# Optimization experiments

Hardware: AMD Instinct MI355X
Metric: run time of the kernel (lower is better)

The kernel has to match this reference:

```python
import jax, jax.numpy as jnp
import numpy as np

NUM_EMBEDDINGS = 1024
EMBEDDING_DIM = 512
B, H, W = 32, 32, 32


def setup_inputs() -> dict:
    key = jax.random.key(0)
    k1, k2 = jax.random.split(key)
    z = jax.random.normal(k1, (B, EMBEDDING_DIM, H, W), dtype=jnp.float32)
    embedding = jax.random.normal(k2, (NUM_EMBEDDINGS, EMBEDDING_DIM), dtype=jnp.float32)
    return {"z": z, "embedding": embedding}


def reference(z, embedding):
    # z: [B, C, H, W] -> [B, H, W, C] -> [N, C]
    zp = jnp.transpose(z, (0, 2, 3, 1))
    b, h, w, d = zp.shape
    z_flat = zp.reshape(-1, d)
    # squared L2 distances: ||z||^2 - 2 z e^T + ||e||^2  -> [N, K]
    distances = (
        jnp.sum(z_flat ** 2, axis=1, keepdims=True)
        - 2.0 * (z_flat @ embedding.T)
        + jnp.sum(embedding ** 2, axis=1)
    )
    indices = jnp.argmin(distances, axis=1)  # [N]
    # one-hot @ embedding == direct gather
    quantized = embedding[indices]  # [N, d]
    quantized = quantized.reshape(b, h, w, d).transpose(0, 3, 1, 2)  # [B, C, H, W]
    return quantized, 0.0, indices.reshape(b, -1)
```

## Files before the change

### kernel.cpp

```cpp
#include <hip/hip_runtime.h>
#include <cfloat>

typedef _Float16 half8 __attribute__((ext_vector_type(8)));
typedef float    f32x4 __attribute__((ext_vector_type(4)));
typedef unsigned int  uint;
typedef unsigned short ushort;

constexpr int DIM  = 512;
constexpr int NEMB = 1024;
constexpr int HW   = 1024;
constexpr int NROW = 32 * HW;

constexpr long long QCOUNT = (long long)32 * 512 * 32 * 32;
constexpr long long SOFF   = QCOUNT;
constexpr long long IOFF   = SOFF + 1;

constexpr size_t WS_ZT    = 0;
constexpr size_t WS_ET    = 33554432;
constexpr size_t WS_ENORM = 34603008;
constexpr size_t WS_CNT   = 34607104;
constexpr size_t WS_LIST  = 34607360;
constexpr size_t WS_CANDB = WS_LIST + (size_t)NROW * 4;
constexpr size_t WS_CANDI = WS_CANDB + (size_t)2 * NROW * 8;
constexpr size_t WS_NEED  = WS_CANDI + (size_t)2 * NROW * 4;

constexpr float DELTA = 0.25f;

__device__ __forceinline__ void gld16(const void* g, void* l) {
    __builtin_amdgcn_global_load_lds(
        (const __attribute__((address_space(1))) void*)g,
        (__attribute__((address_space(3))) void*)l, 16, 0, 0);
}
union PKH8 { half8 v; _Float16 h[8]; };

__device__ __forceinline__ int swz8(int r, int g) {
    return g ^ (r & 7);
}

__global__ __launch_bounds__(256) void prep(const float* __restrict__ z,
                                            const float* __restrict__ e,
                                            char* __restrict__ zt,
                                            char* __restrict__ et,
                                            float* __restrict__ enorm,
                                            int* __restrict__ cnt) {
    __shared__ float ls[64][129];
    const int bx = blockIdx.x;
    const int t  = threadIdx.x;
    if (bx >= 2048) {
        const int eb = bx - 2048;
        if (eb == 0 && t == 0) *cnt = 0;
        int gid = eb * 256 + t;
        int ke  = gid >> 6;
        int kbg = gid & 63;
        const float* src = e + (size_t)ke * DIM + kbg * 8;
        PKH8 h;
        float s = 0.f;
        #pragma unroll
        for (int j = 0; j < 8; ++j) {
            float v = src[j];
            h.h[j] = (_Float16)v;
            s += v * v;
        }
        int nc = ke >> 7, r = ke & 127, kc64 = kbg >> 3, g = kbg & 7;
        size_t byte = ((size_t)(nc * 8 + kc64)) * 16384 + (size_t)r * 128
                    + ((size_t)swz8(r, g) << 4);
        *reinterpret_cast<half8*>(et + byte) = h.v;
        #pragma unroll
        for (int off = 32; off > 0; off >>= 1) s += __shfl_down(s, off, 64);
        if (kbg == 0) enorm[ke] = s;
        return;
    }
    const int mb  = bx >> 3, kcc = bx & 7;
    const int b   = mb >> 3;
    const int hw0 = (mb & 7) * 128;
    for (int i = t; i < 64 * 128; i += 256) {
        int c = i >> 7, hw = i & 127;
        ls[c][hw] = z[((size_t)(b * DIM + kcc * 64 + c)) * HW + hw0 + hw];
    }
    __syncthreads();
    for (int j = t; j < 1024; j += 256) {
        int r = j >> 3, g = j & 7;
        PKH8 h;
        #pragma unroll
        for (int jj = 0; jj < 8; ++jj) h.h[jj] = (_Float16)ls[g * 8 + jj][r];
        size_t byte = ((size_t)(mb * 8 + kcc)) * 16384 + (size_t)r * 128
                    + ((size_t)swz8(r, g) << 4);
        *reinterpret_cast<half8*>(zt + byte) = h.v;
    }
}

#define VQ_STAGE(SS, BUF)                                                      \
  {                                                                            \
    const int kc_ = (SS) & 7;                                                  \
    const size_t tB_ = ((size_t)((half4 + ((SS) >> 3)) * 8 + kc_)) * 16384;    \
    char* dst_ = smem + (BUF) * 32768;                                         \
    gld16(zt + zbase + (size_t)kc_ * 16384 + toff,        dst_ + toff);        \
    gld16(zt + zbase + (size_t)kc_ * 16384 + 8192 + toff, dst_ + 8192 + toff); \
    gld16(et + tB_ + toff,        dst_ + 16384 + toff);                        \
    gld16(et + tB_ + 8192 + toff, dst_ + 24576 + toff);                        \
  }

#define VQ_STEP(S, VMLIT, BUF)                                                 \
  {                                                                            \
    asm volatile("s_waitcnt vmcnt(" VMLIT ")" ::: "memory");                   \
    __builtin_amdgcn_s_barrier();                                              \
    const char* buf_ = smem + (BUF) * 32768;                                   \
    half8 a00 = *reinterpret_cast<const half8*>(buf_ + aoff0);                 \
    half8 a01 = *reinterpret_cast<const half8*>(buf_ + aoff1);                 \
    half8 a10 = *reinterpret_cast<const half8*>(buf_ + (aoff0 ^ 64));          \
    half8 a11 = *reinterpret_cast<const half8*>(buf_ + (aoff1 ^ 64));          \
    half8 b00 = *reinterpret_cast<const half8*>(buf_ + 16384 + boff0);         \
    half8 b01 = *reinterpret_cast<const half8*>(buf_ + 16384 + boff1);         \
    half8 b02 = *reinterpret_cast<const half8*>(buf_ + 16384 + boff2);         \
    half8 b03 = *reinterpret_cast<const half8*>(buf_ + 16384 + boff3);         \
    half8 b10 = *reinterpret_cast<const half8*>(buf_ + 16384 + (boff0 ^ 64));  \
    half8 b11 = *reinterpret_cast<const half8*>(buf_ + 16384 + (boff1 ^ 64));  \
    half8 b12 = *reinterpret_cast<const half8*>(buf_ + 16384 + (boff2 ^ 64));  \
    half8 b13 = *reinterpret_cast<const half8*>(buf_ + 16384 + (boff3 ^ 64));  \
    asm volatile("s_waitcnt lgkmcnt(0)" ::: "memory");                         \
    __builtin_amdgcn_sched_barrier(0);                                         \
    __builtin_amdgcn_s_barrier();                                              \
    if ((S) + 2 < 32) VQ_STAGE((S) + 2, BUF);                                  \
    acc[0][0] = __builtin_amdgcn_mfma_f32_16x16x32_f16(a00, b00, acc[0][0], 0, 0, 0); \
    acc[0][1] = __builtin_amdgcn_mfma_f32_16x16x32_f16(a00, b01, acc[0][1], 0, 0, 0); \
    acc[0][2] = __builtin_amdgcn_mfma_f32_16x16x32_f16(a00, b02, acc[0][2], 0, 0, 0); \
    acc[0][3] = __builtin_amdgcn_mfma_f32_16x16x32_f16(a00, b03, acc[0][3], 0, 0, 0); \
    acc[1][0] = __builtin_amdgcn_mfma_f32_16x16x32_f16(a01, b00, acc[1][0], 0, 0, 0); \
    acc[1][1] = __builtin_amdgcn_mfma_f32_16x16x32_f16(a01, b01, acc[1][1], 0, 0, 0); \
    acc[1][2] = __builtin_amdgcn_mfma_f32_16x16x32_f16(a01, b02, acc[1][2], 0, 0, 0); \
    acc[1][3] = __builtin_amdgcn_mfma_f32_16x16x32_f16(a01, b03, acc[1][3], 0, 0, 0); \
    acc[0][0] = __builtin_amdgcn_mfma_f32_16x16x32_f16(a10, b10, acc[0][0], 0, 0, 0); \
    acc[0][1] = __builtin_amdgcn_mfma_f32_16x16x32_f16(a10, b11, acc[0][1], 0, 0, 0); \
    acc[0][2] = __builtin_amdgcn_mfma_f32_16x16x32_f16(a10, b12, acc[0][2], 0, 0, 0); \
    acc[0][3] = __builtin_amdgcn_mfma_f32_16x16x32_f16(a10, b13, acc[0][3], 0, 0, 0); \
    acc[1][0] = __builtin_amdgcn_mfma_f32_16x16x32_f16(a11, b10, acc[1][0], 0, 0, 0); \
    acc[1][1] = __builtin_amdgcn_mfma_f32_16x16x32_f16(a11, b11, acc[1][1], 0, 0, 0); \
    acc[1][2] = __builtin_amdgcn_mfma_f32_16x16x32_f16(a11, b12, acc[1][2], 0, 0, 0); \
    acc[1][3] = __builtin_amdgcn_mfma_f32_16x16x32_f16(a11, b13, acc[1][3], 0, 0, 0); \
    if (((S) & 7) == 7) {                                                      \
      const int ncl_ = ((S) >> 3) * 128;                                       \
      _Pragma("unroll")                                                        \
      for (int n = 0; n < 4; ++n) {                                            \
        const int lcol = ncl_ + wc * 64 + n * 16 + lr;                         \
        const float en = enorm_l[lcol];                                        \
        const int col = half * 512 + lcol;                                     \
        _Pragma("unroll")                                                      \
        for (int m = 0; m < 2; ++m) {                                          \
          _Pragma("unroll")                                                    \
          for (int q = 0; q < 4; ++q) {                                        \
            float dv = en - 2.0f * acc[m][n][q];                               \
            int sl = m * 4 + q;                                                \
            if (dv < b1v[sl]) { b2v[sl] = b1v[sl]; b1v[sl] = dv; i1v[sl] = col; } \
            else if (dv < b2v[sl]) b2v[sl] = dv;                               \
          }                                                                    \
        }                                                                      \
      }                                                                        \
      _Pragma("unroll")                                                        \
      for (int m = 0; m < 2; ++m)                                              \
        _Pragma("unroll")                                                      \
        for (int n = 0; n < 4; ++n) acc[m][n] = (f32x4)(0.f);                  \
    }                                                                          \
  }

__global__ __launch_bounds__(512, 4) void vq_mfma(const char* __restrict__ zt,
                                                  const char* __restrict__ et,
                                                  const float* __restrict__ enorm,
                                                  float2* __restrict__ cand_b,
                                                  int* __restrict__ cand_i) {
    __shared__ __align__(16) char smem[65536];
    __shared__ float enorm_l[512];

    const int t = threadIdx.x;
    const int w = t >> 6, l = t & 63;
    const int lr = l & 15, hg = l >> 4;
    const int wr = w >> 1;
    const int wc = w & 1;
    const int bid = blockIdx.x;
    const int mb = bid >> 1;
    const int half = bid & 1;
    const int half4 = half * 4;
    const int n0 = mb * 128;

    const int swz = swz8(lr, hg) << 4;
    const int aoff0 = (wr * 32 + lr) * 128 + swz;
    const int aoff1 = (wr * 32 + 16 + lr) * 128 + swz;
    const int boff0 = (wc * 64 + lr) * 128 + swz;
    const int boff1 = (wc * 64 + 16 + lr) * 128 + swz;
    const int boff2 = (wc * 64 + 32 + lr) * 128 + swz;
    const int boff3 = (wc * 64 + 48 + lr) * 128 + swz;

    enorm_l[t] = enorm[half * 512 + t];
    if (t + 256 < 512) enorm_l[t + 256] = enorm[half * 512 + t + 256];
    __syncthreads();

    float b1v[8], b2v[8]; int i1v[8];
    #pragma unroll
    for (int s = 0; s < 8; ++s) { b1v[s] = FLT_MAX; b2v[s] = FLT_MAX; i1v[s] = 0; }

    const size_t zbase = (size_t)mb * 8 * 16384;
    const int toff = t * 16;

    f32x4 acc[2][4];
    #pragma unroll
    for (int m = 0; m < 2; ++m)
        #pragma unroll
        for (int n = 0; n < 4; ++n) acc[m][n] = (f32x4)(0.f);

    VQ_STAGE(0, 0);
    VQ_STAGE(1, 1);

    for (int sp = 0; sp < 30; sp += 2) {
        VQ_STEP(sp + 0, "4", 0);
        VQ_STEP(sp + 1, "4", 1);
    }
    VQ_STEP(30, "4", 0);
    VQ_STEP(31, "0", 1);

    #pragma unroll
    for (int s = 0; s < 8; ++s) {
        #pragma unroll
        for (int off = 1; off <= 8; off <<= 1) {
            float ob1 = __shfl_xor(b1v[s], off, 64);
            int   oi1 = __shfl_xor(i1v[s], off, 64);
            float ob2 = __shfl_xor(b2v[s], off, 64);
            if (ob1 < b1v[s] || (ob1 == b1v[s] && oi1 < i1v[s])) {
                b2v[s] = fminf(b1v[s], ob2);
                b1v[s] = ob1; i1v[s] = oi1;
            } else {
                b2v[s] = fminf(b2v[s], ob1);
            }
        }
    }
    __syncthreads();
    float* red_b1 = reinterpret_cast<float*>(smem);
    float* red_b2 = reinterpret_cast<float*>(smem + 1024);
    int*   red_i1 = reinterpret_cast<int*>  (smem + 2048);
    if (lr == 0) {
        #pragma unroll
        for (int s = 0; s < 8; ++s) {
            int row = wr * 32 + (s >> 2) * 16 + hg * 4 + (s & 3);
            red_b1[row * 2 + wc] = b1v[s];
            red_b2[row * 2 + wc] = b2v[s];
            red_i1[row * 2 + wc] = i1v[s];
        }
    }
    __syncthreads();
    if (t < 128) {
        float a1 = red_b1[t * 2], a2 = red_b2[t * 2]; int ai = red_i1[t * 2];
        float c1 = red_b1[t * 2 + 1], c2 = red_b2[t * 2 + 1]; int ci = red_i1[t * 2 + 1];
        float B1, B2; int I1;
        if (c1 < a1 || (c1 == a1 && ci < ai)) { B1 = c1; I1 = ci; B2 = fminf(a1, c2); }
        else                                   { B1 = a1; I1 = ai; B2 = fminf(a2, c1); }
        cand_b[(size_t)half * NROW + n0 + t] = make_float2(B1, B2);
        cand_i[(size_t)half * NROW + n0 + t] = I1;
    }
}

__global__ __launch_bounds__(256) void combine(const float2* __restrict__ cand_b,
                                               const int* __restrict__ cand_i,
                                               const float* __restrict__ e,
                                               float* __restrict__ out,
                                               int* __restrict__ cnt,
                                               int* __restrict__ list) {
    __shared__ int idx_f[64];
    const int t = threadIdx.x;
    const int n0 = blockIdx.x * 64;
    if (t < 64) {
        const int row = n0 + t;
        float2 a = cand_b[row];
        float2 c = cand_b[NROW + row];
        int ai = cand_i[row];
        int ci = cand_i[NROW + row];
        float B1, B2; int I1;
        if (c.x < a.x) { B1 = c.x; I1 = ci; B2 = fminf(a.x, c.y); }
        else           { B1 = a.x; I1 = ai; B2 = fminf(a.y, c.x); }
        idx_f[t] = I1;
        out[IOFF + row] = (float)I1;
        if (B2 - B1 < DELTA) {
            int pos = atomicAdd(cnt, 1);
            list[pos] = row;
        }
    }
    if (blockIdx.x == 0 && t == 0) out[SOFF] = 0.0f;
    __syncthreads();

    const int b   = n0 >> 10;
    const int hw0 = n0 & (HW - 1);
    const int row4 = (t & 15) * 4;
    const int i0 = idx_f[row4 + 0];
    const int i1 = idx_f[row4 + 1];
    const int i2 = idx_f[row4 + 2];
    const int i3 = idx_f[row4 + 3];
    #pragma unroll 4
    for (int p = 0; p < 32; ++p) {
        int c = (t >> 4) + (p << 4);
        float4 v;
        v.x = e[(size_t)i0 * DIM + c];
        v.y = e[(size_t)i1 * DIM + c];
        v.z = e[(size_t)i2 * DIM + c];
        v.w = e[(size_t)i3 * DIM + c];
        *reinterpret_cast<float4*>(&out[((size_t)(b * DIM + c)) * HW + hw0 + row4]) = v;
    }
}

__global__ __launch_bounds__(256) void recheck(const float* __restrict__ z,
                                               const float* __restrict__ e,
                                               const float* __restrict__ enorm,
                                               const int* __restrict__ cnt,
                                               const int* __restrict__ list,
                                               float* __restrict__ out) {
    __shared__ float zrow[4][512];
    __shared__ float rb[256];
    __shared__ int   ri[256];
    __shared__ int   fidx[4];
    const int t = threadIdx.x;
    const int count = *cnt;
    const int ngrp = (count + 3) >> 2;
    for (int g = blockIdx.x; g < ngrp; g += gridDim.x) {
        const int base = g * 4;
        const int nr = min(4, count - base);
        __syncthreads();
        for (int r = 0; r < nr; ++r) {
            const int row = list[base + r];
            const int b = row >> 10, hw = row & (HW - 1);
            zrow[r][t]       = z[((size_t)(b * DIM + t))       * HW + hw];
            zrow[r][t + 256] = z[((size_t)(b * DIM + t + 256)) * HW + hw];
        }
        __syncthreads();
        float best[4]; int bi[4];
        #pragma unroll
        for (int r = 0; r < 4; ++r) { best[r] = FLT_MAX; bi[r] = 0; }
        #pragma unroll
        for (int p = 0; p < 4; ++p) {
            const int ke = t + p * 256;
            const float4* ep = reinterpret_cast<const float4*>(e + (size_t)ke * DIM);
            float d0 = 0.f, d1 = 0.f, d2 = 0.f, d3 = 0.f;
            const float4* z0 = reinterpret_cast<const float4*>(zrow[0]);
            const float4* z1 = reinterpret_cast<const float4*>(zrow[1]);
            const float4* z2 = reinterpret_cast<const float4*>(zrow[2]);
            const float4* z3 = reinterpret_cast<const float4*>(zrow[3]);
            for (int c = 0; c < 128; ++c) {
                float4 ev = ep[c];
                float4 a0 = z0[c], a1 = z1[c], a2 = z2[c], a3 = z3[c];
                d0 += ev.x*a0.x + ev.y*a0.y + ev.z*a0.z + ev.w*a0.w;
                d1 += ev.x*a1.x + ev.y*a1.y + ev.z*a1.z + ev.w*a1.w;
                d2 += ev.x*a2.x + ev.y*a2.y + ev.z*a2.z + ev.w*a2.w;
                d3 += ev.x*a3.x + ev.y*a3.y + ev.z*a3.z + ev.w*a3.w;
            }
            const float en = enorm[ke];
            float dd[4] = { en - 2.f*d0, en - 2.f*d1, en - 2.f*d2, en - 2.f*d3 };
            #pragma unroll
            for (int r = 0; r < 4; ++r)
                if (dd[r] < best[r]) { best[r] = dd[r]; bi[r] = ke; }
        }
        for (int r = 0; r < nr; ++r) {
            rb[t] = best[r]; ri[t] = bi[r];
            __syncthreads();
            #pragma unroll
            for (int s = 128; s > 0; s >>= 1) {
                if (t < s) {
                    float ov = rb[t + s]; int oi = ri[t + s];
                    if (ov < rb[t] || (ov == rb[t] && oi < ri[t])) {
                        rb[t] = ov; ri[t] = oi;
                    }
                }
                __syncthreads();
            }
            if (t == 0) {
                fidx[r] = ri[0];
                out[IOFF + list[base + r]] = (float)ri[0];
            }
            __syncthreads();
        }
        for (int r = 0; r < nr; ++r) {
            const int row = list[base + r];
            const int b = row >> 10, hw = row & (HW - 1);
            const int fbi = fidx[r];
            out[((size_t)(b * DIM + t))       * HW + hw] = e[(size_t)fbi * DIM + t];
            out[((size_t)(b * DIM + t + 256)) * HW + hw] = e[(size_t)fbi * DIM + t + 256];
        }
    }
}

constexpr int TM = 64;
constexpr int TN = 256;
constexpr int KC = 32;
constexpr int ZST = 68;
constexpr int EST = 260;

union F4 { float4 v; float f[4]; };

__global__ __launch_bounds__(256) void enorm_kernel(const float* __restrict__ e,
                                                    float* __restrict__ enorm) {
    int gid  = blockIdx.x * 256 + threadIdx.x;
    int wave = gid >> 6;
    int lane = gid & 63;
    if (wave >= NEMB) return;
    const float* row = e + (size_t)wave * DIM;
    float4 a = *reinterpret_cast<const float4*>(row + lane * 8);
    float4 b = *reinterpret_cast<const float4*>(row + lane * 8 + 4);
    float s = a.x*a.x + a.y*a.y + a.z*a.z + a.w*a.w
            + b.x*b.x + b.y*b.y + b.z*b.z + b.w*b.w;
    #pragma unroll
    for (int off = 32; off > 0; off >>= 1) s += __shfl_down(s, off, 64);
    if (lane == 0) enorm[wave] = s;
}

__global__ __launch_bounds__(256) void vq_main_kernel(const float* __restrict__ z,
                                                      const float* __restrict__ e,
                                                      const float* __restrict__ enorm,
                                                      float* __restrict__ out) {
    __shared__ float zs[KC][ZST];
    __shared__ float es[KC][EST];
    __shared__ float enorm_l[NEMB];
    __shared__ int   idx_f[TM];

    const int t   = threadIdx.x;
    const int n0  = blockIdx.x * TM;
    const int b   = n0 >> 10;
    const int hw0 = n0 & (HW - 1);
    const float* zb = z + ((size_t)b * DIM) * HW + hw0;

    #pragma unroll
    for (int i = 0; i < 4; ++i) enorm_l[t + i * 256] = enorm[t + i * 256];

    const int rg = t >> 5;
    const int cg = t & 31;

    float best[8];
    int   bidx[8];
    #pragma unroll
    for (int i = 0; i < 8; ++i) { best[i] = FLT_MAX; bidx[i] = 0; }

    const int z_r4 = (t & 15) * 4;
    const int z_c  = t >> 4;
    const int e_ke = t >> 3;
    const int e_c4 = t & 7;

    for (int nc = 0; nc < NEMB / TN; ++nc) {
        const int k0 = nc * TN;
        float acc[8][8];
        #pragma unroll
        for (int mi = 0; mi < 8; ++mi)
            #pragma unroll
            for (int nj = 0; nj < 8; ++nj) acc[mi][nj] = 0.f;

        for (int kc = 0; kc < DIM / KC; ++kc) {
            const int c0 = kc * KC;
            __syncthreads();
            #pragma unroll
            for (int p = 0; p < 2; ++p) {
                int c = z_c + p * 16;
                float4 v = *reinterpret_cast<const float4*>(zb + (size_t)(c0 + c) * HW + z_r4);
                *reinterpret_cast<float4*>(&zs[c][z_r4]) = v;
            }
            #pragma unroll
            for (int p = 0; p < 8; ++p) {
                int ke = e_ke + p * 32;
                float4 v = *reinterpret_cast<const float4*>(e + (size_t)(k0 + ke) * DIM + c0 + e_c4 * 4);
                es[e_c4 * 4 + 0][ke] = v.x;
                es[e_c4 * 4 + 1][ke] = v.y;
                es[e_c4 * 4 + 2][ke] = v.z;
                es[e_c4 * 4 + 3][ke] = v.w;
            }
            __syncthreads();
            #pragma unroll
            for (int kk = 0; kk < KC; ++kk) {
                F4 zf0, zf1, ef0, ef1;
                zf0.v = *reinterpret_cast<const float4*>(&zs[kk][rg * 8]);
                zf1.v = *reinterpret_cast<const float4*>(&zs[kk][rg * 8 + 4]);
                ef0.v = *reinterpret_cast<const float4*>(&es[kk][cg * 4]);
                ef1.v = *reinterpret_cast<const float4*>(&es[kk][128 + cg * 4]);
                #pragma unroll
                for (int mi = 0; mi < 4; ++mi) {
                    #pragma unroll
                    for (int nj = 0; nj < 4; ++nj) {
                        acc[mi][nj]         += zf0.f[mi] * ef0.f[nj];
                        acc[mi][nj + 4]     += zf0.f[mi] * ef1.f[nj];
                        acc[mi + 4][nj]     += zf1.f[mi] * ef0.f[nj];
                        acc[mi + 4][nj + 4] += zf1.f[mi] * ef1.f[nj];
                    }
                }
            }
        }
        #pragma unroll
        for (int mi = 0; mi < 8; ++mi) {
            #pragma unroll
            for (int nj = 0; nj < 8; ++nj) {
                int col = k0 + (nj < 4 ? cg * 4 + nj : 128 + cg * 4 + (nj - 4));
                float dv = enorm_l[col] - 2.0f * acc[mi][nj];
                if (dv < best[mi]) { best[mi] = dv; bidx[mi] = col; }
            }
        }
    }

    __syncthreads();
    float* best_l = reinterpret_cast<float*>(es);
    int*   idx_l  = reinterpret_cast<int*>(reinterpret_cast<char*>(es) + (size_t)TM * 33 * 4);
    #pragma unroll
    for (int mi = 0; mi < 8; ++mi) {
        int row = rg * 8 + mi;
        best_l[row * 33 + cg] = best[mi];
        idx_l[row * 33 + cg]  = bidx[mi];
    }
    __syncthreads();
    if (t < TM) {
        float bv = best_l[t * 33];
        int   bi = idx_l[t * 33];
        #pragma unroll
        for (int c = 1; c < 32; ++c) {
            float v  = best_l[t * 33 + c];
            int   ix = idx_l[t * 33 + c];
            if (v < bv || (v == bv && ix < bi)) { bv = v; bi = ix; }
        }
        idx_f[t] = bi;
        out[IOFF + n0 + t] = (float)bi;
    }
    if (blockIdx.x == 0 && t == 0) out[SOFF] = 0.0f;
    __syncthreads();

    const int row4 = (t & 15) * 4;
    const int i0 = idx_f[row4 + 0];
    const int i1 = idx_f[row4 + 1];
    const int i2 = idx_f[row4 + 2];
    const int i3 = idx_f[row4 + 3];
    #pragma unroll 4
    for (int p = 0; p < 32; ++p) {
        int c = (t >> 4) + (p << 4);
        float4 v;
        v.x = e[(size_t)i0 * DIM + c];
        v.y = e[(size_t)i1 * DIM + c];
        v.z = e[(size_t)i2 * DIM + c];
        v.w = e[(size_t)i3 * DIM + c];
        *reinterpret_cast<float4*>(&out[((size_t)(b * DIM + c)) * HW + hw0 + row4]) = v;
    }
}

extern "C" void kernel_launch(void* const* d_in, const int* in_sizes, int n_in,
                              void* d_out, int out_size, void* d_ws, size_t ws_size,
                              hipStream_t stream) {
    const float* z = (const float*)d_in[0];
    const float* e = (const float*)d_in[1];
    float* out = (float*)d_out;
    char*  ws  = (char*)d_ws;

    if (ws_size >= WS_NEED) {
        char*   zt     = ws + WS_ZT;
        char*   et     = ws + WS_ET;
        float*  enorm  = (float*)(ws + WS_ENORM);
        int*    cnt    = (int*)(ws + WS_CNT);
        int*    list   = (int*)(ws + WS_LIST);
        float2* cand_b = (float2*)(ws + WS_CANDB);
        int*    cand_i = (int*)(ws + WS_CANDI);

        hipLaunchKernelGGL(prep,    dim3(2304),           dim3(256), 0, stream,
                           z, e, zt, et, enorm, cnt);
        hipLaunchKernelGGL(vq_mfma, dim3(NROW / 128 * 2), dim3(512), 0, stream,
                           zt, et, enorm, cand_b, cand_i);
        hipLaunchKernelGGL(combine, dim3(NROW / 64),      dim3(256), 0, stream,
                           cand_b, cand_i, e, out, cnt, list);
        hipLaunchKernelGGL(recheck, dim3(1024),           dim3(256), 0, stream,
                           z, e, enorm, cnt, list, out);
    } else {
        float* enorm = (float*)ws;
        hipLaunchKernelGGL(enorm_kernel,   dim3(NEMB / 4), dim3(256), 0, stream, e, enorm);
        hipLaunchKernelGGL(vq_main_kernel, dim3(NROW / TM), dim3(256), 0, stream,
                           z, e, enorm, out);
    }
}
```

Baseline: 213.8 us.

## Fuse candidate combine into MFMA kernel via last-block atomic handoff

After: 493.9 us. +131.0%, slower.

```diff
diff --git a/kernel.cpp b/kernel.cpp
--- a/kernel.cpp
+++ b/kernel.cpp
@@ -19,7 +19,8 @@
 constexpr size_t WS_ET    = 33554432;
 constexpr size_t WS_ENORM = 34603008;
 constexpr size_t WS_CNT   = 34607104;
-constexpr size_t WS_LIST  = 34607360;
+constexpr size_t WS_READY = 34607360;
+constexpr size_t WS_LIST  = WS_READY + 1024;
 constexpr size_t WS_CANDB = WS_LIST + (size_t)NROW * 4;
 constexpr size_t WS_CANDI = WS_CANDB + (size_t)2 * NROW * 8;
 constexpr size_t WS_NEED  = WS_CANDI + (size_t)2 * NROW * 4;
@@ -42,13 +43,17 @@
                                             char* __restrict__ zt,
                                             char* __restrict__ et,
                                             float* __restrict__ enorm,
-                                            int* __restrict__ cnt) {
+                                            int* __restrict__ cnt,
+                                            int* __restrict__ ready) {
     __shared__ float ls[64][129];
     const int bx = blockIdx.x;
     const int t  = threadIdx.x;
     if (bx >= 2048) {
         const int eb = bx - 2048;
-        if (eb == 0 && t == 0) *cnt = 0;
+        if (eb == 0) {
+            if (t == 0) *cnt = 0;
+            ready[t] = 0;
+        }
         int gid = eb * 256 + t;
         int ke  = gid >> 6;
         int kbg = gid & 63;
@@ -165,10 +170,16 @@
 __global__ __launch_bounds__(512, 4) void vq_mfma(const char* __restrict__ zt,
                                                   const char* __restrict__ et,
                                                   const float* __restrict__ enorm,
+                                                  const float* __restrict__ e,
                                                   float2* __restrict__ cand_b,
-                                                  int* __restrict__ cand_i) {
+                                                  int* __restrict__ cand_i,
+                                                  int* __restrict__ ready,
+                                                  float* __restrict__ out,
+                                                  int* __restrict__ cnt,
+                                                  int* __restrict__ list) {
     __shared__ __align__(16) char smem[65536];
     __shared__ float enorm_l[512];
+    __shared__ int   sflag;
 
     const int t = threadIdx.x;
     const int w = t >> 6, l = t & 63;
@@ -235,6 +246,7 @@
     float* red_b1 = reinterpret_cast<float*>(smem);
     float* red_b2 = reinterpret_cast<float*>(smem + 1024);
     int*   red_i1 = reinterpret_cast<int*>  (smem + 2048);
+    int*   idx_f  = reinterpret_cast<int*>  (smem + 3072);
     if (lr == 0) {
         #pragma unroll
         for (int s = 0; s < 8; ++s) {
@@ -254,51 +266,48 @@
         cand_b[(size_t)half * NROW + n0 + t] = make_float2(B1, B2);
         cand_i[(size_t)half * NROW + n0 + t] = I1;
     }
-}
-
-__global__ __launch_bounds__(256) void combine(const float2* __restrict__ cand_b,
-                                               const int* __restrict__ cand_i,
-                                               const float* __restrict__ e,
-                                               float* __restrict__ out,
-                                               int* __restrict__ cnt,
-                                               int* __restrict__ list) {
-    __shared__ int idx_f[64];
-    const int t = threadIdx.x;
-    const int n0 = blockIdx.x * 64;
-    if (t < 64) {
-        const int row = n0 + t;
-        float2 a = cand_b[row];
-        float2 c = cand_b[NROW + row];
-        int ai = cand_i[row];
-        int ci = cand_i[NROW + row];
+    if (mb == 0 && half == 0 && t == 0) out[SOFF] = 0.0f;
+
+    __threadfence();
+    __syncthreads();
+    if (t == 0) sflag = atomicAdd(&ready[mb], 1);
+    __syncthreads();
+    if (sflag == 0) return;
+    __threadfence();
+
+    if (t < 128) {
+        float2 a = cand_b[n0 + t];
+        float2 c = cand_b[NROW + n0 + t];
+        int ai = cand_i[n0 + t];
+        int ci = cand_i[NROW + n0 + t];
         float B1, B2; int I1;
         if (c.x < a.x) { B1 = c.x; I1 = ci; B2 = fminf(a.x, c.y); }
         else           { B1 = a.x; I1 = ai; B2 = fminf(a.y, c.x); }
         idx_f[t] = I1;
-        out[IOFF + row] = (float)I1;
+        out[IOFF + n0 + t] = (float)I1;
         if (B2 - B1 < DELTA) {
             int pos = atomicAdd(cnt, 1);
-            list[pos] = row;
-        }
-    }
-    if (blockIdx.x == 0 && t == 0) out[SOFF] = 0.0f;
-    __syncthreads();
-
-    const int b   = n0 >> 10;
-    const int hw0 = n0 & (HW - 1);
-    const int row4 = (t & 15) * 4;
+            list[pos] = n0 + t;
+        }
+    }
+    __syncthreads();
+
+    const int b   = mb >> 3;
+    const int hw0 = (mb & 7) * 128;
+    const int row4 = (t & 31) * 4;
     const int i0 = idx_f[row4 + 0];
-    const int i1 = idx_f[row4 + 1];
+    const int i1g = idx_f[row4 + 1];
     const int i2 = idx_f[row4 + 2];
     const int i3 = idx_f[row4 + 3];
+    const int cbase = t >> 5;
     #pragma unroll 4
     for (int p = 0; p < 32; ++p) {
-        int c = (t >> 4) + (p << 4);
+        int c = cbase + (p << 4);
         float4 v;
-        v.x = e[(size_t)i0 * DIM + c];
-        v.y = e[(size_t)i1 * DIM + c];
-        v.z = e[(size_t)i2 * DIM + c];
-        v.w = e[(size_t)i3 * DIM + c];
+        v.x = e[(size_t)i0  * DIM + c];
+        v.y = e[(size_t)i1g * DIM + c];
+        v.z = e[(size_t)i2  * DIM + c];
+        v.w = e[(size_t)i3  * DIM + c];
         *reinterpret_cast<float4*>(&out[((size_t)(b * DIM + c)) * HW + hw0 + row4]) = v;
     }
 }
@@ -309,16 +318,16 @@
                                                const int* __restrict__ cnt,
                                                const int* __restrict__ list,
                                                float* __restrict__ out) {
-    __shared__ float zrow[4][512];
+    __shared__ float zrow[8][512];
     __shared__ float rb[256];
     __shared__ int   ri[256];
-    __shared__ int   fidx[4];
+    __shared__ int   fidx[8];
     const int t = threadIdx.x;
     const int count = *cnt;
-    const int ngrp = (count + 3) >> 2;
+    const int ngrp = (count + 7) >> 3;
     for (int g = blockIdx.x; g < ngrp; g += gridDim.x) {
-        const int base = g * 4;
-        const int nr = min(4, count - base);
+        const int base = g * 8;
+        const int nr = min(8, count - base);
         __syncthreads();
         for (int r = 0; r < nr; ++r) {
             const int row = list[base + r];
@@ -327,50 +336,80 @@
             zrow[r][t + 256] = z[((size_t)(b * DIM + t + 256)) * HW + hw];
         }
         __syncthreads();
-        float best[4]; int bi[4];
-        #pragma unroll
-        for (int r = 0; r < 4; ++r) { best[r] = FLT_MAX; bi[r] = 0; }
+        float best0 = FLT_MAX, best1 = FLT_MAX, best2 = FLT_MAX, best3 = FLT_MAX;
+        float best4 = FLT_MAX, best5 = FLT_MAX, best6 = FLT_MAX, best7 = FLT_MAX;
+        int bi0 = 0, bi1 = 0, bi2 = 0, bi3 = 0, bi4 = 0, bi5 = 0, bi6 = 0, bi7 = 0;
         #pragma unroll
         for (int p = 0; p < 4; ++p) {
             const int ke = t + p * 256;
             const float4* ep = reinterpret_cast<const float4*>(e + (size_t)ke * DIM);
             float d0 = 0.f, d1 = 0.f, d2 = 0.f, d3 = 0.f;
+            float d4 = 0.f, d5 = 0.f, d6 = 0.f, d7 = 0.f;
             const float4* z0 = reinterpret_cast<const float4*>(zrow[0]);
             const float4* z1 = reinterpret_cast<const float4*>(zrow[1]);
             const float4* z2 = reinterpret_cast<const float4*>(zrow[2]);
             const float4* z3 = reinterpret_cast<const float4*>(zrow[3]);
+            const float4* z4 = reinterpret_cast<const float4*>(zrow[4]);
+            const float4* z5 = reinterpret_cast<const float4*>(zrow[5]);
+            const float4* z6 = reinterpret_cast<const float4*>(zrow[6]);
+            const float4* z7 = reinterpret_cast<const float4*>(zrow[7]);
             for (int c = 0; c < 128; ++c) {
                 float4 ev = ep[c];
                 float4 a0 = z0[c], a1 = z1[c], a2 = z2[c], a3 = z3[c];
+                float4 a4 = z4[c], a5 = z5[c], a6 = z6[c], a7 = z7[c];
                 d0 += ev.x*a0.x + ev.y*a0.y + ev.z*a0.z + ev.w*a0.w;
                 d1 += ev.x*a1.x + ev.y*a1.y + ev.z*a1.z + ev.w*a1.w;
                 d2 += ev.x*a2.x + ev.y*a2.y + ev.z*a2.z + ev.w*a2.w;
                 d3 += ev.x*a3.x + ev.y*a3.y + ev.z*a3.z + ev.w*a3.w;
+                d4 += ev.x*a4.x + ev.y*a4.y + ev.z*a4.z + ev.w*a4.w;
+                d5 += ev.x*a5.x + ev.y*a5.y + ev.z*a5.z + ev.w*a5.w;
+                d6 += ev.x*a6.x + ev.y*a6.y + ev.z*a6.z + ev.w*a6.w;
+                d7 += ev.x*a7.x + ev.y*a7.y + ev.z*a7.z + ev.w*a7.w;
             }
             const float en = enorm[ke];
-            float dd[4] = { en - 2.f*d0, en - 2.f*d1, en - 2.f*d2, en - 2.f*d3 };
-            #pragma unroll
-            for (int r = 0; r < 4; ++r)
-                if (dd[r] < best[r]) { best[r] = dd[r]; bi[r] = ke; }
-        }
-        for (int r = 0; r < nr; ++r) {
-            rb[t] = best[r]; ri[t] = bi[r];
-            __syncthreads();
-            #pragma unroll
-            for (int s = 128; s > 0; s >>= 1) {
-                if (t < s) {
-                    float ov = rb[t + s]; int oi = ri[t + s];
-                    if (ov < rb[t] || (ov == rb[t] && oi < ri[t])) {
-                        rb[t] = ov; ri[t] = oi;
+            float v0 = en - 2.f*d0, v1 = en - 2.f*d1, v2 = en - 2.f*d2, v3 = en - 2.f*d3;
+            float v4 = en - 2.f*d4, v5 = en - 2.f*d5, v6 = en - 2.f*d6, v7 = en - 2.f*d7;
+            if (v0 < best0) { best0 = v0; bi0 = ke; }
+            if (v1 < best1) { best1 = v1; bi1 = ke; }
+            if (v2 < best2) { best2 = v2; bi2 = ke; }
+            if (v3 < best3) { best3 = v3; bi3 = ke; }
+            if (v4 < best4) { best4 = v4; bi4 = ke; }
+            if (v5 < best5) { best5 = v5; bi5 = ke; }
+            if (v6 < best6) { best6 = v6; bi6 = ke; }
+            if (v7 < best7) { best7 = v7; bi7 = ke; }
+        }
+        #pragma unroll
+        for (int r = 0; r < 8; ++r) {
+            if (r < nr) {
+                float bv; int bix;
+                switch (r) {
+                    case 0: bv = best0; bix = bi0; break;
+                    case 1: bv = best1; bix = bi1; break;
+                    case 2: bv = best2; bix = bi2; break;
+                    case 3: bv = best3; bix = bi3; break;
+                    case 4: bv = best4; bix = bi4; break;
+                    case 5: bv = best5; bix = bi5; break;
+                    case 6: bv = best6; bix = bi6; break;
+                    default: bv = best7; bix = bi7; break;
+                }
+                rb[t] = bv; ri[t] = bix;
+                __syncthreads();
+                #pragma unroll
+                for (int s = 128; s > 0; s >>= 1) {
+                    if (t < s) {
+                        float ov = rb[t + s]; int oi = ri[t + s];
+                        if (ov < rb[t] || (ov == rb[t] && oi < ri[t])) {
+                            rb[t] = ov; ri[t] = oi;
+                        }
                     }
+                    __syncthreads();
+                }
+                if (t == 0) {
+                    fidx[r] = ri[0];
+                    out[IOFF + list[base + r]] = (float)ri[0];
                 }
                 __syncthreads();
             }
-            if (t == 0) {
-                fidx[r] = ri[0];
-                out[IOFF + list[base + r]] = (float)ri[0];
-            }
-            __syncthreads();
         }
         for (int r = 0; r < nr; ++r) {
             const int row = list[base + r];
@@ -549,16 +588,15 @@
         char*   et     = ws + WS_ET;
         float*  enorm  = (float*)(ws + WS_ENORM);
         int*    cnt    = (int*)(ws + WS_CNT);
+        int*    ready  = (int*)(ws + WS_READY);
         int*    list   = (int*)(ws + WS_LIST);
         float2* cand_b = (float2*)(ws + WS_CANDB);
         int*    cand_i = (int*)(ws + WS_CANDI);
 
         hipLaunchKernelGGL(prep,    dim3(2304),           dim3(256), 0, stream,
-                           z, e, zt, et, enorm, cnt);
+                           z, e, zt, et, enorm, cnt, ready);
         hipLaunchKernelGGL(vq_mfma, dim3(NROW / 128 * 2), dim3(512), 0, stream,
-                           zt, et, enorm, cand_b, cand_i);
-        hipLaunchKernelGGL(combine, dim3(NROW / 64),      dim3(256), 0, stream,
-                           cand_b, cand_i, e, out, cnt, list);
+                           zt, et, enorm, e, cand_b, cand_i, ready, out, cnt, list);
         hipLaunchKernelGGL(recheck, dim3(1024),           dim3(256), 0, stream,
                            z, e, enorm, cnt, list, out);
     } else {
```
